# Optimization experiments

Hardware: AMD Instinct MI355X
Metric: run time of the kernel (lower is better)

## Reference

```python
import jax, jax.numpy as jnp
import numpy as np

B, S, H = 64, 1024, 1000

def setup_inputs() -> dict:
    key = jax.random.key(0)
    k1, k2, k3, k4 = jax.random.split(key, 4)
    h_tgt = jax.random.normal(k1, (B, 1, H), dtype=jnp.float32)
    h_src = jax.random.normal(k2, (B, S, H), dtype=jnp.float32)
    # nn.Linear(H, H) params: weight [H, H], bias [H]
    bound = 1.0 / np.sqrt(H)
    W = jax.random.uniform(k3, (H, H), dtype=jnp.float32, minval=-bound, maxval=bound)
    b = jax.random.uniform(k4, (H,), dtype=jnp.float32, minval=-bound, maxval=bound)
    return {"h_tgt": h_tgt, "h_src": h_src, "W": W, "b": b}

def reference(h_tgt, h_src, W, b):
    # score[b,t] = h_tgt[b,0] . (W @ h_src[b,t] + bias)  -- Luong general attention
    proj = jnp.einsum('bsh,gh->bsg', h_src, W) + b          # [B,S,H]
    score = jnp.einsum('bh,bsh->bs', h_tgt[:, 0], proj)      # [B,S]
    a = jax.nn.softmax(score, axis=1)                        # [B,S]
    c = jnp.einsum('bs,bsh->bh', a, h_src)[:, None, :]       # [B,1,H]
    return c
```

## Files before the change

kernel.cpp:

```cpp
#include <hip/hip_runtime.h>

typedef float v4f __attribute__((ext_vector_type(4)));

constexpr int Bb = 64;
constexpr int Ss = 1024;
constexpr int Hh = 1000;
constexpr int CHUNKS = 32;
constexpr int CS = Ss / CHUNKS;
constexpr int BG = 4;
constexpr int GS = 8;
constexpr int GL = Hh / GS;

__global__ __launch_bounds__(64) void proj_tgt_kernel(
    const float* __restrict__ h_tgt, const float* __restrict__ W,
    float* __restrict__ u_part)
{
    const int lane = (int)threadIdx.x;
    const int b0   = (int)blockIdx.x * BG;
    const int slot = (int)blockIdx.y * 64 + lane;
    const int p    = (int)blockIdx.z;
    const bool ok  = (slot < Hh / 4);
    const int h    = slot * 4;

    v4f acc[BG];
    #pragma unroll
    for (int bi = 0; bi < BG; ++bi) acc[bi] = (v4f){0.f, 0.f, 0.f, 0.f};

    const float* wp = W + (size_t)(p * GL) * Hh + h;
    const int gbase = p * GL;
    #pragma unroll 4
    for (int g = 0; g < GL; ++g) {
        const v4f w4 = ok ? *(const v4f*)wp : (v4f){0.f, 0.f, 0.f, 0.f};
        #pragma unroll
        for (int bi = 0; bi < BG; ++bi) {
            const float a = h_tgt[(b0 + bi) * Hh + gbase + g];
            acc[bi] += a * w4;
        }
        wp += Hh;
    }
    if (ok) {
        #pragma unroll
        for (int bi = 0; bi < BG; ++bi)
            *(v4f*)(u_part + (size_t)(p * Bb + b0 + bi) * Hh + h) = acc[bi];
    }
}

__global__ __launch_bounds__(256) void ureduce_kernel(
    const float* __restrict__ u_part, float* __restrict__ u)
{
    const int i = (int)(blockIdx.x * blockDim.x + threadIdx.x);
    if (i < Bb * Hh / 4) {
        v4f s = (v4f){0.f, 0.f, 0.f, 0.f};
        #pragma unroll
        for (int p = 0; p < GS; ++p)
            s += *(const v4f*)(u_part + (size_t)p * Bb * Hh + i * 4);
        *(v4f*)(u + i * 4) = s;
    }
}

__global__ __launch_bounds__(256) void attn_partial_kernel(
    const float* __restrict__ h_src, const float* __restrict__ u,
    float* __restrict__ wsM, float* __restrict__ wsL, float* __restrict__ wsC)
{
    const int lane  = threadIdx.x & 63;
    const int wave  = (int)((blockIdx.x * blockDim.x + threadIdx.x) >> 6);
    const int b     = wave >> 5;
    const int chunk = wave & 31;
    const int s0    = chunk * CS;

    const float* ub = u + b * Hh;
    v4f uf[4];
    #pragma unroll
    for (int j = 0; j < 4; ++j) {
        const int d = j * 256 + lane * 4;
        uf[j] = (d < Hh) ? *(const v4f*)(ub + d) : (v4f){0.f, 0.f, 0.f, 0.f};
    }

    float m = -INFINITY, l = 0.f;
    v4f c[4];
    #pragma unroll
    for (int j = 0; j < 4; ++j) c[j] = (v4f){0.f, 0.f, 0.f, 0.f};

    const float* xp = h_src + (size_t)(b * Ss + s0) * Hh;
    for (int s = 0; s < CS; s += 4) {
        v4f x[4][4];
        #pragma unroll
        for (int r = 0; r < 4; ++r) {
            #pragma unroll
            for (int j = 0; j < 4; ++j) {
                const int d = j * 256 + lane * 4;
                x[r][j] = (d < Hh)
                    ? __builtin_nontemporal_load((const v4f*)(xp + (size_t)r * Hh + d))
                    : (v4f){0.f, 0.f, 0.f, 0.f};
            }
        }
        float p[4] = {0.f, 0.f, 0.f, 0.f};
        #pragma unroll
        for (int r = 0; r < 4; ++r) {
            #pragma unroll
            for (int j = 0; j < 4; ++j) {
                p[r] = fmaf(x[r][j].x, uf[j].x, p[r]);
                p[r] = fmaf(x[r][j].y, uf[j].y, p[r]);
                p[r] = fmaf(x[r][j].z, uf[j].z, p[r]);
                p[r] = fmaf(x[r][j].w, uf[j].w, p[r]);
            }
        }
        #pragma unroll
        for (int off = 32; off > 0; off >>= 1) {
            #pragma unroll
            for (int r = 0; r < 4; ++r) p[r] += __shfl_xor(p[r], off, 64);
        }

        const float mx01 = fmaxf(p[0], p[1]);
        const float mx23 = fmaxf(p[2], p[3]);
        const float mn = fmaxf(m, fmaxf(mx01, mx23));
        if (mn > m) {
            const float scale = __expf(m - mn);
            m = mn;
            l *= scale;
            #pragma unroll
            for (int j = 0; j < 4; ++j) c[j] *= scale;
        }
        float e[4];
        #pragma unroll
        for (int r = 0; r < 4; ++r) e[r] = __expf(p[r] - m);
        l += (e[0] + e[1]) + (e[2] + e[3]);
        #pragma unroll
        for (int r = 0; r < 4; ++r) {
            #pragma unroll
            for (int j = 0; j < 4; ++j) {
                c[j].x = fmaf(e[r], x[r][j].x, c[j].x);
                c[j].y = fmaf(e[r], x[r][j].y, c[j].y);
                c[j].z = fmaf(e[r], x[r][j].z, c[j].z);
                c[j].w = fmaf(e[r], x[r][j].w, c[j].w);
            }
        }
        xp += 4 * Hh;
    }

    const int idx = b * CHUNKS + chunk;
    if (lane == 0) { wsM[idx] = m; wsL[idx] = l; }
    float* cw = wsC + (size_t)idx * Hh;
    #pragma unroll
    for (int j = 0; j < 4; ++j) {
        const int d = j * 256 + lane * 4;
        if (d < Hh) *(v4f*)(cw + d) = c[j];
    }
}

__global__ __launch_bounds__(256) void combine_kernel(
    const float* __restrict__ wsM, const float* __restrict__ wsL,
    const float* __restrict__ wsC, float* __restrict__ out)
{
    const int b   = blockIdx.x;
    const int tid = (int)threadIdx.x;
    __shared__ float sw[CHUNKS];
    __shared__ float sInvL;

    if (tid < 64) {
        const bool v = (tid < CHUNKS);
        const float mi = v ? wsM[b * CHUNKS + tid] : -INFINITY;
        const float li = v ? wsL[b * CHUNKS + tid] : 0.f;
        float M = mi;
        #pragma unroll
        for (int off = 32; off > 0; off >>= 1) M = fmaxf(M, __shfl_xor(M, off, 64));
        const float w = __expf(mi - M);
        float L = w * li;
        #pragma unroll
        for (int off = 32; off > 0; off >>= 1) L += __shfl_xor(L, off, 64);
        if (v) sw[tid] = w;
        if (tid == 0) sInvL = 1.f / L;
    }
    __syncthreads();

    const int h = tid * 4;
    if (h < Hh) {
        v4f acc = (v4f){0.f, 0.f, 0.f, 0.f};
        #pragma unroll 8
        for (int i = 0; i < CHUNKS; ++i)
            acc += sw[i] * *(const v4f*)(wsC + (size_t)(b * CHUNKS + i) * Hh + h);
        *(v4f*)(out + b * Hh + h) = acc * sInvL;
    }
}

extern "C" void kernel_launch(void* const* d_in, const int* in_sizes, int n_in,
                              void* d_out, int out_size, void* d_ws, size_t ws_size,
                              hipStream_t stream) {
    const float* h_tgt = (const float*)d_in[0];
    const float* h_src = (const float*)d_in[1];
    const float* W     = (const float*)d_in[2];
    float* out = (float*)d_out;

    float* u      = (float*)d_ws;
    float* wsM    = u + Bb * Hh;
    float* wsL    = wsM + Bb * CHUNKS;
    float* wsC    = wsL + Bb * CHUNKS;
    float* u_part = wsC + (size_t)Bb * CHUNKS * Hh;

    proj_tgt_kernel<<<dim3(Bb / BG, 4, GS), 64, 0, stream>>>(h_tgt, W, u_part);
    ureduce_kernel<<<(Bb * Hh / 4 + 255) / 256, 256, 0, stream>>>(u_part, u);
    attn_partial_kernel<<<(Bb * CHUNKS) / 4, 256, 0, stream>>>(h_src, u, wsM, wsL, wsC);
    combine_kernel<<<Bb, 256, 0, stream>>>(wsM, wsL, wsC, out);
}
```

Before: 377.6 us.

## Fold split-K reduction of target projection into LDS and split combine across blocks

The target projection kernel now puts its 8 K-slices in waves of one 512-thread block and sums the partial results in shared memory, so the separate ureduce kernel and the u_part round trip through global memory go away. Each thread now handles 2 output columns instead of 4, over 8 column groups. The combine kernel is also split into two 128-thread blocks per batch for more parallelism. This saves one launch and some global traffic. In exchange it adds a block barrier and narrower loads in the projection.

```diff
diff --git a/kernel.cpp b/kernel.cpp
--- a/kernel.cpp
+++ b/kernel.cpp
@@ -1,6 +1,7 @@
 #include <hip/hip_runtime.h>
 
 typedef float v4f __attribute__((ext_vector_type(4)));
+typedef float v2f __attribute__((ext_vector_type(2)));
 
 constexpr int Bb = 64;
 constexpr int Ss = 1024;
@@ -8,53 +9,48 @@
 constexpr int CHUNKS = 32;
 constexpr int CS = Ss / CHUNKS;
 constexpr int BG = 4;
-constexpr int GS = 8;
-constexpr int GL = Hh / GS;
-
-__global__ __launch_bounds__(64) void proj_tgt_kernel(
+constexpr int PW = 8;
+constexpr int GL = Hh / PW;
+
+__global__ __launch_bounds__(512) void proj_tgt_kernel(
     const float* __restrict__ h_tgt, const float* __restrict__ W,
-    float* __restrict__ u_part)
+    float* __restrict__ u)
 {
-    const int lane = (int)threadIdx.x;
+    const int tid  = (int)threadIdx.x;
+    const int lane = tid & 63;
+    const int w    = tid >> 6;
     const int b0   = (int)blockIdx.x * BG;
     const int slot = (int)blockIdx.y * 64 + lane;
-    const int p    = (int)blockIdx.z;
-    const bool ok  = (slot < Hh / 4);
-    const int h    = slot * 4;
-
-    v4f acc[BG];
-    #pragma unroll
-    for (int bi = 0; bi < BG; ++bi) acc[bi] = (v4f){0.f, 0.f, 0.f, 0.f};
-
-    const float* wp = W + (size_t)(p * GL) * Hh + h;
-    const int gbase = p * GL;
+    const bool ok  = (slot < Hh / 2);
+    const int h    = slot * 2;
+
+    v2f acc[BG];
+    #pragma unroll
+    for (int bi = 0; bi < BG; ++bi) acc[bi] = (v2f){0.f, 0.f};
+
+    const int gbase = w * GL;
+    const float* wp = W + (size_t)gbase * Hh + h;
     #pragma unroll 4
     for (int g = 0; g < GL; ++g) {
-        const v4f w4 = ok ? *(const v4f*)wp : (v4f){0.f, 0.f, 0.f, 0.f};
+        const v2f w2 = ok ? *(const v2f*)wp : (v2f){0.f, 0.f};
         #pragma unroll
         for (int bi = 0; bi < BG; ++bi) {
             const float a = h_tgt[(b0 + bi) * Hh + gbase + g];
-            acc[bi] += a * w4;
+            acc[bi] += a * w2;
         }
         wp += Hh;
     }
-    if (ok) {
-        #pragma unroll
-        for (int bi = 0; bi < BG; ++bi)
-            *(v4f*)(u_part + (size_t)(p * Bb + b0 + bi) * Hh + h) = acc[bi];
-    }
-}
-
-__global__ __launch_bounds__(256) void ureduce_kernel(
-    const float* __restrict__ u_part, float* __restrict__ u)
-{
-    const int i = (int)(blockIdx.x * blockDim.x + threadIdx.x);
-    if (i < Bb * Hh / 4) {
-        v4f s = (v4f){0.f, 0.f, 0.f, 0.f};
-        #pragma unroll
-        for (int p = 0; p < GS; ++p)
-            s += *(const v4f*)(u_part + (size_t)p * Bb * Hh + i * 4);
-        *(v4f*)(u + i * 4) = s;
+
+    __shared__ v2f red[BG][PW][64];
+    #pragma unroll
+    for (int bi = 0; bi < BG; ++bi) red[bi][w][lane] = acc[bi];
+    __syncthreads();
+
+    if (w < BG) {
+        v2f s = red[w][0][lane];
+        #pragma unroll
+        for (int p = 1; p < PW; ++p) s += red[w][p][lane];
+        if (ok) *(v2f*)(u + (size_t)(b0 + w) * Hh + h) = s;
     }
 }
 
@@ -148,12 +144,13 @@
     }
 }
 
-__global__ __launch_bounds__(256) void combine_kernel(
+__global__ __launch_bounds__(128) void combine_kernel(
     const float* __restrict__ wsM, const float* __restrict__ wsL,
     const float* __restrict__ wsC, float* __restrict__ out)
 {
-    const int b   = blockIdx.x;
-    const int tid = (int)threadIdx.x;
+    const int b    = (int)blockIdx.x;
+    const int half = (int)blockIdx.y;
+    const int tid  = (int)threadIdx.x;
     __shared__ float sw[CHUNKS];
     __shared__ float sInvL;
 
@@ -173,8 +170,9 @@
     }
     __syncthreads();
 
-    const int h = tid * 4;
-    if (h < Hh) {
+    const int slot = half * 125 + tid;
+    if (tid < 125) {
+        const int h = slot * 4;
         v4f acc = (v4f){0.f, 0.f, 0.f, 0.f};
         #pragma unroll 8
         for (int i = 0; i < CHUNKS; ++i)
@@ -191,14 +189,12 @@
     const float* W     = (const float*)d_in[2];
     float* out = (float*)d_out;
 
-    float* u      = (float*)d_ws;
-    float* wsM    = u + Bb * Hh;
-    float* wsL    = wsM + Bb * CHUNKS;
-    float* wsC    = wsL + Bb * CHUNKS;
-    float* u_part = wsC + (size_t)Bb * CHUNKS * Hh;
-
-    proj_tgt_kernel<<<dim3(Bb / BG, 4, GS), 64, 0, stream>>>(h_tgt, W, u_part);
-    ureduce_kernel<<<(Bb * Hh / 4 + 255) / 256, 256, 0, stream>>>(u_part, u);
+    float* u   = (float*)d_ws;
+    float* wsM = u + Bb * Hh;
+    float* wsL = wsM + Bb * CHUNKS;
+    float* wsC = wsL + Bb * CHUNKS;
+
+    proj_tgt_kernel<<<dim3(Bb / BG, 8), 512, 0, stream>>>(h_tgt, W, u);
     attn_partial_kernel<<<(Bb * CHUNKS) / 4, 256, 0, stream>>>(h_src, u, wsM, wsL, wsC);
-    combine_kernel<<<Bb, 256, 0, stream>>>(wsM, wsL, wsC, out);
-}
+    combine_kernel<<<dim3(Bb, 2), 128, 0, stream>>>(wsM, wsL, wsC, out);
+}
```

Result: no change. 373.2 us (-1.2%).
